# Kernel optimization log

Measured on AMD Instinct MI355X. Metric: run time of the kernel, lower is better.

Reference implementation:

```python
import jax, jax.numpy as jnp
import numpy as np
import math

B, S = 2, 2048
D_IN = 512
D_OUT = 512
P = 8
K = 8


def setup_inputs() -> dict:
    key = jax.random.key(0)
    ks = jax.random.split(key, 8)
    mean_phi = math.log(math.sqrt(2.0 / (D_IN * K)))
    mean_w2 = math.log(math.sqrt(2.0 / D_OUT))
    x = jax.random.normal(ks[0], (B, S, D_IN), dtype=jnp.float32)
    phi_raw = mean_phi + 0.2 * jax.random.normal(ks[1], (D_OUT, D_IN * K), dtype=jnp.float32)
    phi_bias = jnp.zeros((D_OUT,), dtype=jnp.float32)
    raw_weight2 = mean_w2 + 0.2 * jax.random.normal(ks[2], (P, D_OUT, D_OUT), dtype=jnp.float32)
    bias2 = jnp.zeros((P, D_OUT), dtype=jnp.float32)
    gate_raw2 = jnp.full((P,), -3.0, dtype=jnp.float32)
    # kaiming_uniform with a=sqrt(5) on shape (P, 2*D_in, D_out): fan_in = 2*D_in
    bound = math.sqrt(6.0 / ((1.0 + 5.0) * (2 * D_IN)))
    z_weight = jax.random.uniform(ks[3], (P, 2 * D_IN, D_OUT), dtype=jnp.float32,
                                  minval=-bound, maxval=bound)
    gate_raw = jnp.full((P,), -3.0, dtype=jnp.float32)
    output_bias = jnp.zeros((P, D_OUT), dtype=jnp.float32)
    return {
        "x": x, "phi_raw": phi_raw, "phi_bias": phi_bias,
        "raw_weight2": raw_weight2, "bias2": bias2, "gate_raw2": gate_raw2,
        "z_weight": z_weight, "gate_raw": gate_raw, "output_bias": output_bias,
    }


def reference(x, phi_raw, phi_bias, raw_weight2, bias2, gate_raw2,
              z_weight, gate_raw, output_bias):
    sp = jax.nn.softplus
    orig = x.shape
    x_flat = x.reshape(-1, D_IN)                              # [N, Din]
    N = x_flat.shape[0]
    shifts = jnp.linspace(-1.0, 1.0, K, dtype=x.dtype)        # [k]
    phi = sp(x_flat[:, :, None] + shifts[None, None, :])      # [N, Din, k]
    phi_flat = phi.reshape(N, D_IN * K)                       # [N, Din*k]
    # PositiveLinearHK: weight = softplus(raw)^2
    w_phi = jnp.square(sp(phi_raw))                           # [Dout, Din*k]
    x_proj = phi_flat @ w_phi.T + phi_bias                    # [N, Dout]
    g1 = jax.nn.sigmoid(gate_raw)[:, None, None]              # [P,1,1]
    z0 = sp(x_proj[None, :, :] * g1)                          # [P, N, Dout]
    w2 = jnp.square(sp(raw_weight2))                          # [P, Dout, Dout]
    # bmm(z0, w2.transpose(1,2)) == einsum over the second Dout axis of w2
    z1 = jnp.einsum('pnd,ped->pne', z0, w2) + bias2[:, None, :]
    g2 = jax.nn.sigmoid(gate_raw2)[:, None, None]
    z1 = sp(z1 * g2)                                          # [P, N, Dout]
    x_res_in = jnp.concatenate([x_flat, x_flat], axis=-1)     # [N, 2*Din]
    x_res = jnp.einsum('nc,pce->pne', x_res_in, z_weight)     # [P, N, Dout]
    z_final = sp(z1 + x_res) + output_bias[:, None, :]        # [P, N, Dout]
    out = jnp.transpose(z_final, (1, 0, 2))                   # [N, P, Dout]
    return out.reshape(tuple(orig[:-1]) + (P, D_OUT))
```

## Files before the change

### kernel.cpp

```cpp
#include <hip/hip_runtime.h>

typedef unsigned short u16;
typedef __attribute__((ext_vector_type(8))) short bf16x8;
typedef __attribute__((ext_vector_type(4))) float floatx4;
typedef __attribute__((ext_vector_type(8))) unsigned short u16x8;
typedef __attribute__((ext_vector_type(4))) unsigned short u16x4;

#define NTOK 4096
#define DDIN 512
#define DDOUT 512
#define NP 8

__device__ __forceinline__ u16 f2b(float f) {
    union { float f; unsigned int u; } v; v.f = f;
    unsigned int r = (v.u + 0x7fffu + ((v.u >> 16) & 1u)) >> 16;
    return (u16)r;
}
__device__ __forceinline__ float sp(float x) {
    return fmaxf(x, 0.f) + __logf(1.f + __expf(-fabsf(x)));
}
__device__ __forceinline__ float sigm(float x) { return 1.f / (1.f + __expf(-x)); }

__device__ __forceinline__ void gld16(const u16* g, u16* l) {
    __builtin_amdgcn_global_load_lds((const __attribute__((address_space(1))) void*)g,
                                     (__attribute__((address_space(3))) void*)l, 16, 0, 0);
}

__global__ void prep_sqsp(const float* __restrict__ in, u16* __restrict__ out, int n) {
    int i = blockIdx.x * 256 + threadIdx.x;
    if (i < n) {
        float s = sp(in[i]);
        out[i] = f2b(s * s);
    }
}

__global__ void prep_zwT(const float* __restrict__ zw, u16* __restrict__ zwT) {
    int p = blockIdx.z;
    int c0 = blockIdx.x * 32, e0 = blockIdx.y * 32;
    __shared__ float tb[32][33];
    int tx = threadIdx.x, ty = threadIdx.y;
    const float* base = zw + (size_t)p * 1024 * 512;
#pragma unroll
    for (int r = 0; r < 4; ++r) {
        int cl = ty * 4 + r;
        float a = base[(size_t)(c0 + cl) * 512 + e0 + tx];
        float b = base[(size_t)(c0 + cl + 512) * 512 + e0 + tx];
        tb[cl][tx] = a + b;
    }
    __syncthreads();
    u16* outb = zwT + (size_t)p * 512 * 512;
#pragma unroll
    for (int r = 0; r < 4; ++r) {
        int el = ty * 4 + r;
        outb[(size_t)(e0 + el) * 512 + c0 + tx] = f2b(tb[tx][el]);
    }
}

__global__ void phi_kernel(const float* __restrict__ x, u16* __restrict__ phi,
                           u16* __restrict__ xb) {
    int i = blockIdx.x * 256 + threadIdx.x;
    float xv = x[i];
    xb[i] = f2b(xv);
    u16x8 v;
#pragma unroll
    for (int k = 0; k < 8; ++k) {
        float s = -1.f + (2.f / 7.f) * (float)k;
        v[k] = f2b(sp(xv + s));
    }
    *(u16x8*)(phi + (size_t)i * 8) = v;
}

__launch_bounds__(256, 2)
__global__ void gemm1p(const u16* __restrict__ phi, const u16* __restrict__ wphi,
                       float* __restrict__ xpart) {
    __shared__ __align__(16) u16 lds[2 * 8192];
    u16* As = lds;
    u16* Bs = lds + 8192;

    const int id = blockIdx.x;
    const int xcd = id & 7, local = id >> 3;
    const int kc = xcd & 3, nh = xcd >> 2;
    const int o0 = (local & 3) * 128;
    const int n0 = (nh * 16 + (local >> 2)) * 128;
    const int kbase = kc * 1024;

    const int t = threadIdx.x;
    const int wave = t >> 6, lane = t & 63;
    const int wm = wave >> 1, wn = wave & 1;
    const int l15 = lane & 15, quad = lane >> 4;
    const int srow = t >> 3, scol = (t & 7) * 8;

    floatx4 acc[4][4];
#pragma unroll
    for (int i = 0; i < 4; ++i)
#pragma unroll
        for (int j = 0; j < 4; ++j) acc[i][j] = {0.f, 0.f, 0.f, 0.f};

    for (int k0 = 0; k0 < 1024; k0 += 64) {
        const u16* ga = phi + (size_t)(n0 + srow) * 4096 + kbase + k0 + scol;
        const u16* gb = wphi + (size_t)(o0 + srow) * 4096 + kbase + k0 + scol;
        __syncthreads();
#pragma unroll
        for (int c = 0; c < 4; ++c) {
            gld16(ga + (size_t)c * 32 * 4096, As + c * 2048 + t * 8);
            gld16(gb + (size_t)c * 32 * 4096, Bs + c * 2048 + t * 8);
        }
        __syncthreads();
#pragma unroll
        for (int ks = 0; ks < 2; ++ks) {
            bf16x8 a[4], b[4];
#pragma unroll
            for (int s = 0; s < 4; ++s) {
                a[s] = *(const bf16x8*)(As + (wm * 64 + s * 16 + l15) * 64 + ks * 32 + quad * 8);
                b[s] = *(const bf16x8*)(Bs + (wn * 64 + s * 16 + l15) * 64 + ks * 32 + quad * 8);
            }
#pragma unroll
            for (int sm = 0; sm < 4; ++sm)
#pragma unroll
                for (int sn = 0; sn < 4; ++sn)
                    acc[sm][sn] = __builtin_amdgcn_mfma_f32_16x16x32_bf16(a[sm], b[sn], acc[sm][sn], 0, 0, 0);
        }
    }

    float* xp = xpart + (size_t)kc * NTOK * DDOUT;
#pragma unroll
    for (int sm = 0; sm < 4; ++sm)
#pragma unroll
        for (int sn = 0; sn < 4; ++sn) {
            int gcol = o0 + wn * 64 + sn * 16 + l15;
#pragma unroll
            for (int r = 0; r < 4; ++r) {
                int grow = n0 + wm * 64 + sm * 16 + quad * 4 + r;
                xp[(size_t)grow * DDOUT + gcol] = acc[sm][sn][r];
            }
        }
}

__global__ void reduce_ep(const float* __restrict__ xpart, const float* __restrict__ phi_bias,
                          const float* __restrict__ gate_raw, u16* __restrict__ z0) {
    int idx = blockIdx.x * 256 + threadIdx.x;
    int n = idx >> 7;
    int o4 = (idx & 127) * 4;
    size_t base = (size_t)n * DDOUT + o4;
    floatx4 s = *(const floatx4*)(xpart + base);
#pragma unroll
    for (int kc = 1; kc < 4; ++kc) {
        floatx4 v = *(const floatx4*)(xpart + (size_t)kc * NTOK * DDOUT + base);
        s[0] += v[0]; s[1] += v[1]; s[2] += v[2]; s[3] += v[3];
    }
    floatx4 pb = *(const floatx4*)(phi_bias + o4);
    s[0] += pb[0]; s[1] += pb[1]; s[2] += pb[2]; s[3] += pb[3];
#pragma unroll
    for (int p = 0; p < NP; ++p) {
        float g = sigm(gate_raw[p]);
        u16x4 v;
        v[0] = f2b(sp(s[0] * g)); v[1] = f2b(sp(s[1] * g));
        v[2] = f2b(sp(s[2] * g)); v[3] = f2b(sp(s[3] * g));
        *(u16x4*)(z0 + (size_t)p * NTOK * DDOUT + base) = v;
    }
}

__launch_bounds__(256, 2)
__global__ void gemm23(const u16* __restrict__ z0, const u16* __restrict__ w2b,
                       const u16* __restrict__ xb, const u16* __restrict__ zwT,
                       const float* __restrict__ bias2, const float* __restrict__ gate_raw2,
                       const float* __restrict__ output_bias, float* __restrict__ out) {
    __shared__ __align__(16) u16 lds[4 * 8192];
    u16* A1 = lds;
    u16* B1 = lds + 8192;
    u16* A2 = lds + 16384;
    u16* B2 = lds + 24576;

    const int id = blockIdx.x;
    const int p = id & 7;
    const int local = id >> 3;
    const int e0 = (local & 3) * 128;
    const int n0 = (local >> 2) * 128;

    const int t = threadIdx.x;
    const int wave = t >> 6, lane = t & 63;
    const int wm = wave >> 1, wn = wave & 1;
    const int l15 = lane & 15, quad = lane >> 4;
    const int srow = t >> 3, scol = (t & 7) * 8;

    const u16* z0p = z0 + (size_t)p * NTOK * DDOUT;
    const u16* w2p = w2b + (size_t)p * DDOUT * DDOUT;
    const u16* zwp = zwT + (size_t)p * DDOUT * DDIN;

    floatx4 acc1[4][4], acc2[4][4];
#pragma unroll
    for (int i = 0; i < 4; ++i)
#pragma unroll
        for (int j = 0; j < 4; ++j) {
            acc1[i][j] = {0.f, 0.f, 0.f, 0.f};
            acc2[i][j] = {0.f, 0.f, 0.f, 0.f};
        }

    for (int k0 = 0; k0 < 512; k0 += 64) {
        const u16* ga1 = z0p + (size_t)(n0 + srow) * 512 + k0 + scol;
        const u16* gb1 = w2p + (size_t)(e0 + srow) * 512 + k0 + scol;
        const u16* ga2 = xb  + (size_t)(n0 + srow) * 512 + k0 + scol;
        const u16* gb2 = zwp + (size_t)(e0 + srow) * 512 + k0 + scol;
        __syncthreads();
#pragma unroll
        for (int c = 0; c < 4; ++c) {
            gld16(ga1 + (size_t)c * 32 * 512, A1 + c * 2048 + t * 8);
            gld16(gb1 + (size_t)c * 32 * 512, B1 + c * 2048 + t * 8);
            gld16(ga2 + (size_t)c * 32 * 512, A2 + c * 2048 + t * 8);
            gld16(gb2 + (size_t)c * 32 * 512, B2 + c * 2048 + t * 8);
        }
        __syncthreads();
#pragma unroll
        for (int ks = 0; ks < 2; ++ks) {
            bf16x8 a1[4], b1[4], a2[4], b2[4];
#pragma unroll
            for (int s = 0; s < 4; ++s) {
                int ro = (wm * 64 + s * 16 + l15) * 64 + ks * 32 + quad * 8;
                int co = (wn * 64 + s * 16 + l15) * 64 + ks * 32 + quad * 8;
                a1[s] = *(const bf16x8*)(A1 + ro);
                b1[s] = *(const bf16x8*)(B1 + co);
                a2[s] = *(const bf16x8*)(A2 + ro);
                b2[s] = *(const bf16x8*)(B2 + co);
            }
#pragma unroll
            for (int sm = 0; sm < 4; ++sm)
#pragma unroll
                for (int sn = 0; sn < 4; ++sn) {
                    acc1[sm][sn] = __builtin_amdgcn_mfma_f32_16x16x32_bf16(a1[sm], b1[sn], acc1[sm][sn], 0, 0, 0);
                    acc2[sm][sn] = __builtin_amdgcn_mfma_f32_16x16x32_bf16(a2[sm], b2[sn], acc2[sm][sn], 0, 0, 0);
                }
        }
    }

    const float g2p = sigm(gate_raw2[p]);
#pragma unroll
    for (int sm = 0; sm < 4; ++sm)
#pragma unroll
        for (int sn = 0; sn < 4; ++sn) {
            int gcol = e0 + wn * 64 + sn * 16 + l15;
            float bb = bias2[p * DDOUT + gcol];
            float ob = output_bias[p * DDOUT + gcol];
#pragma unroll
            for (int r = 0; r < 4; ++r) {
                int grow = n0 + wm * 64 + sm * 16 + quad * 4 + r;
                float v1 = acc1[sm][sn][r] + bb;
                float o = sp(sp(v1 * g2p) + acc2[sm][sn][r]) + ob;
                out[(size_t)grow * (NP * DDOUT) + p * DDOUT + gcol] = o;
            }
        }
}

extern "C" void kernel_launch(void* const* d_in, const int* in_sizes, int n_in,
                              void* d_out, int out_size, void* d_ws, size_t ws_size,
                              hipStream_t stream) {
    const float* x           = (const float*)d_in[0];
    const float* phi_raw     = (const float*)d_in[1];
    const float* phi_bias    = (const float*)d_in[2];
    const float* raw_weight2 = (const float*)d_in[3];
    const float* bias2       = (const float*)d_in[4];
    const float* gate_raw2   = (const float*)d_in[5];
    const float* z_weight    = (const float*)d_in[6];
    const float* gate_raw    = (const float*)d_in[7];
    const float* output_bias = (const float*)d_in[8];
    float* out = (float*)d_out;

    u16* ws   = (u16*)d_ws;
    u16* phi  = ws;
    u16* wphi = phi + (size_t)4096 * 4096;
    u16* w2b  = wphi + (size_t)512 * 4096;
    u16* zwT  = w2b + (size_t)8 * 512 * 512;
    u16* z0   = zwT + (size_t)8 * 512 * 512;
    u16* xb   = z0 + (size_t)8 * 4096 * 512;
    float* xpart = (float*)d_out;

    hipLaunchKernelGGL(prep_sqsp, dim3(8192), dim3(256), 0, stream, phi_raw, wphi, 512 * 4096);
    hipLaunchKernelGGL(prep_sqsp, dim3(8192), dim3(256), 0, stream, raw_weight2, w2b, 8 * 512 * 512);
    hipLaunchKernelGGL(prep_zwT, dim3(16, 16, 8), dim3(32, 8), 0, stream, z_weight, zwT);
    hipLaunchKernelGGL(phi_kernel, dim3(8192), dim3(256), 0, stream, x, phi, xb);
    hipLaunchKernelGGL(gemm1p, dim3(512), dim3(256), 0, stream, phi, wphi, xpart);
    hipLaunchKernelGGL(reduce_ep, dim3(2048), dim3(256), 0, stream, xpart, phi_bias, gate_raw, z0);
    hipLaunchKernelGGL(gemm23, dim3(1024), dim3(256), 0, stream,
                       z0, w2b, xb, zwT, bias2, gate_raw2, output_bias, out);
}
```

Before: 224.8 us.

## Split gemm1 K eight ways with bf16 partials and halve gemm23 K tile

```diff
diff --git a/kernel.cpp b/kernel.cpp
--- a/kernel.cpp
+++ b/kernel.cpp
@@ -11,6 +11,9 @@
 #define DDOUT 512
 #define NP 8
 
+__device__ __forceinline__ float b2f(u16 b) {
+    union { unsigned int u; float f; } v; v.u = ((unsigned int)b) << 16; return v.f;
+}
 __device__ __forceinline__ u16 f2b(float f) {
     union { float f; unsigned int u; } v; v.f = f;
     unsigned int r = (v.u + 0x7fffu + ((v.u >> 16) & 1u)) >> 16;
@@ -70,19 +73,19 @@
     *(u16x8*)(phi + (size_t)i * 8) = v;
 }
 
-__launch_bounds__(256, 2)
+__launch_bounds__(256, 4)
 __global__ void gemm1p(const u16* __restrict__ phi, const u16* __restrict__ wphi,
-                       float* __restrict__ xpart) {
+                       u16* __restrict__ xpart) {
     __shared__ __align__(16) u16 lds[2 * 8192];
     u16* As = lds;
     u16* Bs = lds + 8192;
 
     const int id = blockIdx.x;
-    const int xcd = id & 7, local = id >> 3;
-    const int kc = xcd & 3, nh = xcd >> 2;
+    const int kc = id & 7;
+    const int local = id >> 3;
     const int o0 = (local & 3) * 128;
-    const int n0 = (nh * 16 + (local >> 2)) * 128;
-    const int kbase = kc * 1024;
+    const int n0 = (local >> 2) * 128;
+    const int kbase = kc * 512;
 
     const int t = threadIdx.x;
     const int wave = t >> 6, lane = t & 63;
@@ -96,7 +99,7 @@
 #pragma unroll
         for (int j = 0; j < 4; ++j) acc[i][j] = {0.f, 0.f, 0.f, 0.f};
 
-    for (int k0 = 0; k0 < 1024; k0 += 64) {
+    for (int k0 = 0; k0 < 512; k0 += 64) {
         const u16* ga = phi + (size_t)(n0 + srow) * 4096 + kbase + k0 + scol;
         const u16* gb = wphi + (size_t)(o0 + srow) * 4096 + kbase + k0 + scol;
         __syncthreads();
@@ -122,7 +125,7 @@
         }
     }
 
-    float* xp = xpart + (size_t)kc * NTOK * DDOUT;
+    u16* xp = xpart + (size_t)kc * NTOK * DDOUT;
 #pragma unroll
     for (int sm = 0; sm < 4; ++sm)
 #pragma unroll
@@ -131,45 +134,45 @@
 #pragma unroll
             for (int r = 0; r < 4; ++r) {
                 int grow = n0 + wm * 64 + sm * 16 + quad * 4 + r;
-                xp[(size_t)grow * DDOUT + gcol] = acc[sm][sn][r];
-            }
-        }
-}
-
-__global__ void reduce_ep(const float* __restrict__ xpart, const float* __restrict__ phi_bias,
+                xp[(size_t)grow * DDOUT + gcol] = f2b(acc[sm][sn][r]);
+            }
+        }
+}
+
+__global__ void reduce_ep(const u16* __restrict__ xpart, const float* __restrict__ phi_bias,
                           const float* __restrict__ gate_raw, u16* __restrict__ z0) {
     int idx = blockIdx.x * 256 + threadIdx.x;
     int n = idx >> 7;
     int o4 = (idx & 127) * 4;
     size_t base = (size_t)n * DDOUT + o4;
-    floatx4 s = *(const floatx4*)(xpart + base);
-#pragma unroll
-    for (int kc = 1; kc < 4; ++kc) {
-        floatx4 v = *(const floatx4*)(xpart + (size_t)kc * NTOK * DDOUT + base);
-        s[0] += v[0]; s[1] += v[1]; s[2] += v[2]; s[3] += v[3];
+    float s0 = 0.f, s1 = 0.f, s2 = 0.f, s3 = 0.f;
+#pragma unroll
+    for (int kc = 0; kc < 8; ++kc) {
+        u16x4 v = *(const u16x4*)(xpart + (size_t)kc * NTOK * DDOUT + base);
+        s0 += b2f(v[0]); s1 += b2f(v[1]); s2 += b2f(v[2]); s3 += b2f(v[3]);
     }
     floatx4 pb = *(const floatx4*)(phi_bias + o4);
-    s[0] += pb[0]; s[1] += pb[1]; s[2] += pb[2]; s[3] += pb[3];
+    s0 += pb[0]; s1 += pb[1]; s2 += pb[2]; s3 += pb[3];
 #pragma unroll
     for (int p = 0; p < NP; ++p) {
         float g = sigm(gate_raw[p]);
         u16x4 v;
-        v[0] = f2b(sp(s[0] * g)); v[1] = f2b(sp(s[1] * g));
-        v[2] = f2b(sp(s[2] * g)); v[3] = f2b(sp(s[3] * g));
+        v[0] = f2b(sp(s0 * g)); v[1] = f2b(sp(s1 * g));
+        v[2] = f2b(sp(s2 * g)); v[3] = f2b(sp(s3 * g));
         *(u16x4*)(z0 + (size_t)p * NTOK * DDOUT + base) = v;
     }
 }
 
-__launch_bounds__(256, 2)
+__launch_bounds__(256, 4)
 __global__ void gemm23(const u16* __restrict__ z0, const u16* __restrict__ w2b,
                        const u16* __restrict__ xb, const u16* __restrict__ zwT,
                        const float* __restrict__ bias2, const float* __restrict__ gate_raw2,
                        const float* __restrict__ output_bias, float* __restrict__ out) {
-    __shared__ __align__(16) u16 lds[4 * 8192];
+    __shared__ __align__(16) u16 lds[4 * 4096];
     u16* A1 = lds;
-    u16* B1 = lds + 8192;
-    u16* A2 = lds + 16384;
-    u16* B2 = lds + 24576;
+    u16* B1 = lds + 4096;
+    u16* A2 = lds + 8192;
+    u16* B2 = lds + 12288;
 
     const int id = blockIdx.x;
     const int p = id & 7;
@@ -181,7 +184,7 @@
     const int wave = t >> 6, lane = t & 63;
     const int wm = wave >> 1, wn = wave & 1;
     const int l15 = lane & 15, quad = lane >> 4;
-    const int srow = t >> 3, scol = (t & 7) * 8;
+    const int srow = t >> 2, scol = (t & 3) * 8;
 
     const u16* z0p = z0 + (size_t)p * NTOK * DDOUT;
     const u16* w2p = w2b + (size_t)p * DDOUT * DDOUT;
@@ -196,40 +199,37 @@
             acc2[i][j] = {0.f, 0.f, 0.f, 0.f};
         }
 
-    for (int k0 = 0; k0 < 512; k0 += 64) {
+    for (int k0 = 0; k0 < 512; k0 += 32) {
         const u16* ga1 = z0p + (size_t)(n0 + srow) * 512 + k0 + scol;
         const u16* gb1 = w2p + (size_t)(e0 + srow) * 512 + k0 + scol;
         const u16* ga2 = xb  + (size_t)(n0 + srow) * 512 + k0 + scol;
         const u16* gb2 = zwp + (size_t)(e0 + srow) * 512 + k0 + scol;
         __syncthreads();
 #pragma unroll
-        for (int c = 0; c < 4; ++c) {
-            gld16(ga1 + (size_t)c * 32 * 512, A1 + c * 2048 + t * 8);
-            gld16(gb1 + (size_t)c * 32 * 512, B1 + c * 2048 + t * 8);
-            gld16(ga2 + (size_t)c * 32 * 512, A2 + c * 2048 + t * 8);
-            gld16(gb2 + (size_t)c * 32 * 512, B2 + c * 2048 + t * 8);
-        }
-        __syncthreads();
-#pragma unroll
-        for (int ks = 0; ks < 2; ++ks) {
-            bf16x8 a1[4], b1[4], a2[4], b2[4];
-#pragma unroll
-            for (int s = 0; s < 4; ++s) {
-                int ro = (wm * 64 + s * 16 + l15) * 64 + ks * 32 + quad * 8;
-                int co = (wn * 64 + s * 16 + l15) * 64 + ks * 32 + quad * 8;
-                a1[s] = *(const bf16x8*)(A1 + ro);
-                b1[s] = *(const bf16x8*)(B1 + co);
-                a2[s] = *(const bf16x8*)(A2 + ro);
-                b2[s] = *(const bf16x8*)(B2 + co);
-            }
-#pragma unroll
-            for (int sm = 0; sm < 4; ++sm)
-#pragma unroll
-                for (int sn = 0; sn < 4; ++sn) {
-                    acc1[sm][sn] = __builtin_amdgcn_mfma_f32_16x16x32_bf16(a1[sm], b1[sn], acc1[sm][sn], 0, 0, 0);
-                    acc2[sm][sn] = __builtin_amdgcn_mfma_f32_16x16x32_bf16(a2[sm], b2[sn], acc2[sm][sn], 0, 0, 0);
-                }
-        }
+        for (int c = 0; c < 2; ++c) {
+            gld16(ga1 + (size_t)c * 64 * 512, A1 + c * 2048 + t * 8);
+            gld16(gb1 + (size_t)c * 64 * 512, B1 + c * 2048 + t * 8);
+            gld16(ga2 + (size_t)c * 64 * 512, A2 + c * 2048 + t * 8);
+            gld16(gb2 + (size_t)c * 64 * 512, B2 + c * 2048 + t * 8);
+        }
+        __syncthreads();
+        bf16x8 a1[4], b1[4], a2[4], b2[4];
+#pragma unroll
+        for (int s = 0; s < 4; ++s) {
+            int ro = (wm * 64 + s * 16 + l15) * 32 + quad * 8;
+            int co = (wn * 64 + s * 16 + l15) * 32 + quad * 8;
+            a1[s] = *(const bf16x8*)(A1 + ro);
+            b1[s] = *(const bf16x8*)(B1 + co);
+            a2[s] = *(const bf16x8*)(A2 + ro);
+            b2[s] = *(const bf16x8*)(B2 + co);
+        }
+#pragma unroll
+        for (int sm = 0; sm < 4; ++sm)
+#pragma unroll
+            for (int sn = 0; sn < 4; ++sn) {
+                acc1[sm][sn] = __builtin_amdgcn_mfma_f32_16x16x32_bf16(a1[sm], b1[sn], acc1[sm][sn], 0, 0, 0);
+                acc2[sm][sn] = __builtin_amdgcn_mfma_f32_16x16x32_bf16(a2[sm], b2[sn], acc2[sm][sn], 0, 0, 0);
+            }
     }
 
     const float g2p = sigm(gate_raw2[p]);
@@ -271,13 +271,13 @@
     u16* zwT  = w2b + (size_t)8 * 512 * 512;
     u16* z0   = zwT + (size_t)8 * 512 * 512;
     u16* xb   = z0 + (size_t)8 * 4096 * 512;
-    float* xpart = (float*)d_out;
+    u16* xpart = (u16*)d_out;
 
     hipLaunchKernelGGL(prep_sqsp, dim3(8192), dim3(256), 0, stream, phi_raw, wphi, 512 * 4096);
     hipLaunchKernelGGL(prep_sqsp, dim3(8192), dim3(256), 0, stream, raw_weight2, w2b, 8 * 512 * 512);
     hipLaunchKernelGGL(prep_zwT, dim3(16, 16, 8), dim3(32, 8), 0, stream, z_weight, zwT);
     hipLaunchKernelGGL(phi_kernel, dim3(8192), dim3(256), 0, stream, x, phi, xb);
-    hipLaunchKernelGGL(gemm1p, dim3(512), dim3(256), 0, stream, phi, wphi, xpart);
+    hipLaunchKernelGGL(gemm1p, dim3(1024), dim3(256), 0, stream, phi, wphi, xpart);
     hipLaunchKernelGGL(reduce_ep, dim3(2048), dim3(256), 0, stream, xpart, phi_bias, gate_raw, z0);
     hipLaunchKernelGGL(gemm23, dim3(1024), dim3(256), 0, stream,
                        z0, w2b, xb, zwT, bias2, gate_raw2, output_bias, out);
```

Result: slower. 498.0 us (+121.5%).
